# Performance work log

Hardware: AMD Instinct MI355X
Metric: run time of the kernel (lower is better)

The kernel has to match this reference:

```python
import jax, jax.numpy as jnp
import numpy as np

B, L, D = 8, 1024, 512
H, DK, DV = 8, 64, 64
DLAT = 512

def _ln(x, g, b, eps):
    m = jnp.mean(x, axis=-1, keepdims=True)
    var = jnp.mean((x - m) ** 2, axis=-1, keepdims=True)
    return (x - m) * jax.lax.rsqrt(var + eps) * g + b

def setup_inputs() -> dict:
    key = jax.random.key(0)
    ks = jax.random.split(key, 16)
    s = lambda fan: 1.0 / np.sqrt(fan)
    inp = {
        "q": jax.random.normal(ks[0], (B, L, D), jnp.float32),
        "k": jax.random.normal(ks[1], (B, L, D), jnp.float32),
        "v": jax.random.normal(ks[2], (B, L, D), jnp.float32),
        "latent": jax.random.normal(ks[3], (B, 1, DLAT), jnp.float32),
        "Wq": jax.random.normal(ks[4], (D, H * DK), jnp.float32) * s(D),
        "bq": jnp.zeros((H * DK,), jnp.float32),
        "Wk": jax.random.normal(ks[5], (D, H * DK), jnp.float32) * s(D),
        "bk": jnp.zeros((H * DK,), jnp.float32),
        "Wv": jax.random.normal(ks[6], (D, H * DV), jnp.float32) * s(D),
        "bv": jnp.zeros((H * DV,), jnp.float32),
        "Wfc": jax.random.normal(ks[7], (H * DV, D), jnp.float32) * s(H * DV),
        "bfc": jnp.zeros((D,), jnp.float32),
        "Ws1": jax.random.normal(ks[8], (DLAT, 2 * D), jnp.float32) * s(DLAT),
        "bs1": jnp.zeros((2 * D,), jnp.float32),
        "Ws2": jax.random.normal(ks[9], (D, D), jnp.float32) * s(D),
        "bs2": jnp.zeros((D,), jnp.float32),
        "en_g": jnp.ones((D,), jnp.float32),
        "en_b": jnp.zeros((D,), jnp.float32),
        "ln_g": jnp.ones((D,), jnp.float32),
        "ln_b": jnp.zeros((D,), jnp.float32),
    }
    return inp

def reference(q, k, v, latent, Wq, bq, Wk, bk, Wv, bv, Wfc, bfc, Ws1, bs1, Ws2, bs2, en_g, en_b, ln_g, ln_b):
    residual = q
    # QKV projections -> [B, L, H, d]
    Q = (q @ Wq + bq).reshape(B, L, H, DK)
    K = (k @ Wk + bk).reshape(B, L, H, DK)
    V = (v @ Wv + bv).reshape(B, L, H, DV)
    # scaled dot-product attention (dropout = identity in eval)
    scores = jnp.einsum("bqhd,bkhd->bhqk", Q, K) / jnp.sqrt(jnp.float32(DK))
    attn = jax.nn.softmax(scores, axis=-1)
    o = jnp.einsum("bhqk,bkhd->bqhd", attn, V).reshape(B, L, H * DV)
    o = o @ Wfc + bfc
    # ScaledStylizationBlock (FiLM): SiLU -> Linear -> split scale/shift
    lat = jax.nn.silu(latent) @ Ws1 + bs1          # [B, 1, 2D]
    scale, shift = jnp.split(lat, 2, axis=2)
    h = _ln(o, en_g, en_b, 1e-5) * (1.0 + scale) + shift
    h = jax.nn.silu(h) @ Ws2 + bs2
    out = _ln(h + residual, ln_g, ln_b, 1e-6)
    return out, attn
```

## Files before the change

### kernel.cpp

```cpp
#include <hip/hip_runtime.h>
#include <hip/hip_bf16.h>
#include <math.h>

#define BB 8
#define LLEN 1024
#define DDIM 512
#define HH 8
#define DLAT 512
#define NROW (BB * LLEN)
#define ROWELEM 4194304

typedef __bf16 bf16x8 __attribute__((ext_vector_type(8)));
typedef __bf16 bf16x4 __attribute__((ext_vector_type(4)));
typedef float  f32x4  __attribute__((ext_vector_type(4)));

__device__ inline __bf16 f2bf(float f) {
    union { float f; unsigned u; } a; a.f = f;
    unsigned r = (a.u + 0x7fffu + ((a.u >> 16) & 1u)) >> 16;
    union { unsigned short s; __bf16 b; } o; o.s = (unsigned short)r;
    return o.b;
}

__global__ __launch_bounds__(256) void wtrans_kernel(
    const float* __restrict__ W, __bf16* __restrict__ WT)
{
    __shared__ float t[64][65];
    const int tid = threadIdx.x;
    const int bx = blockIdx.x & 7;
    const int by = blockIdx.x >> 3;
    const int r0 = by * 64, c0 = bx * 64;

    #pragma unroll
    for (int p = 0; p < 4; ++p) {
        int r = p * 16 + (tid >> 4);
        int c = (tid & 15) * 4;
        f32x4 v = *(const f32x4*)(W + (size_t)(r0 + r) * 512 + c0 + c);
        t[r][c] = v[0]; t[r][c + 1] = v[1]; t[r][c + 2] = v[2]; t[r][c + 3] = v[3];
    }
    __syncthreads();
    #pragma unroll
    for (int p = 0; p < 4; ++p) {
        int c = p * 16 + (tid >> 4);
        int rc = (tid & 15) * 4;
        bf16x4 o;
        #pragma unroll
        for (int m = 0; m < 4; ++m) o[m] = f2bf(t[rc + m][c]);
        *(bf16x4*)(WT + (size_t)(c0 + c) * 512 + r0 + rc) = o;
    }
}

__global__ __launch_bounds__(256) void wtrans_hilo_kernel(
    const float* __restrict__ W, __bf16* __restrict__ WTh, __bf16* __restrict__ WTl)
{
    __shared__ float t[64][65];
    const int tid = threadIdx.x;
    const int bx = blockIdx.x & 7;
    const int by = blockIdx.x >> 3;
    const int r0 = by * 64, c0 = bx * 64;

    #pragma unroll
    for (int p = 0; p < 4; ++p) {
        int r = p * 16 + (tid >> 4);
        int c = (tid & 15) * 4;
        f32x4 v = *(const f32x4*)(W + (size_t)(r0 + r) * 512 + c0 + c);
        t[r][c] = v[0]; t[r][c + 1] = v[1]; t[r][c + 2] = v[2]; t[r][c + 3] = v[3];
    }
    __syncthreads();
    #pragma unroll
    for (int p = 0; p < 4; ++p) {
        int c = p * 16 + (tid >> 4);
        int rc = (tid & 15) * 4;
        bf16x4 oh, ol;
        #pragma unroll
        for (int m = 0; m < 4; ++m) {
            float v = t[rc + m][c];
            __bf16 hi = f2bf(v);
            oh[m] = hi;
            ol[m] = f2bf(v - (float)hi);
        }
        *(bf16x4*)(WTh + (size_t)(c0 + c) * 512 + r0 + rc) = oh;
        *(bf16x4*)(WTl + (size_t)(c0 + c) * 512 + r0 + rc) = ol;
    }
}

__global__ __launch_bounds__(256) void gemm_qkv_mfma(
    const float* __restrict__ A, const __bf16* __restrict__ Bt,
    const float* __restrict__ bias, __bf16* __restrict__ C)
{
    const int tid  = threadIdx.x;
    const int w    = tid >> 6, lane = tid & 63;
    const int quad = lane >> 4, lid = lane & 15;
    const int wm = w >> 1, wn = w & 1;
    const int col0 = blockIdx.x * 64;
    const int row0 = blockIdx.y * 128;

    __shared__ __bf16 As[128][72];
    __shared__ __bf16 Bs[64][72];

    const f32x4 zero = {0.f, 0.f, 0.f, 0.f};
    f32x4 acc[4][2];
    #pragma unroll
    for (int i = 0; i < 4; ++i)
        #pragma unroll
        for (int j = 0; j < 2; ++j) acc[i][j] = zero;

    for (int kt = 0; kt < 512; kt += 64) {
        __syncthreads();
        {
            const int rr = lane >> 4;
            const int cc = lane & 15;
            #pragma unroll
            for (int p = 0; p < 8; ++p) {
                int r = w * 32 + p * 4 + rr;
                f32x4 v = *(const f32x4*)(A + (size_t)(row0 + r) * 512 + kt + cc * 4);
                bf16x4 o;
                #pragma unroll
                for (int m = 0; m < 4; ++m) o[m] = f2bf(v[m]);
                *(bf16x4*)&As[r][cc * 4] = o;
            }
        }
        {
            const int rr = lane >> 3;
            const int cc = lane & 7;
            #pragma unroll
            for (int p = 0; p < 2; ++p) {
                int r = w * 16 + p * 8 + rr;
                *(bf16x8*)&Bs[r][cc * 8] =
                    *(const bf16x8*)(Bt + (size_t)(col0 + r) * 512 + kt + cc * 8);
            }
        }
        __syncthreads();
        #pragma unroll
        for (int ks = 0; ks < 2; ++ks) {
            bf16x8 a[4], b[2];
            #pragma unroll
            for (int i = 0; i < 4; ++i)
                a[i] = *(const bf16x8*)&As[wm * 64 + i * 16 + lid][ks * 32 + quad * 8];
            #pragma unroll
            for (int j = 0; j < 2; ++j)
                b[j] = *(const bf16x8*)&Bs[wn * 32 + j * 16 + lid][ks * 32 + quad * 8];
            #pragma unroll
            for (int i = 0; i < 4; ++i)
                #pragma unroll
                for (int j = 0; j < 2; ++j)
                    acc[i][j] = __builtin_amdgcn_mfma_f32_16x16x32_bf16(a[i], b[j], acc[i][j], 0, 0, 0);
        }
    }

    float bcol[2];
    #pragma unroll
    for (int j = 0; j < 2; ++j) bcol[j] = bias[col0 + wn * 32 + j * 16 + lid];
    #pragma unroll
    for (int i = 0; i < 4; ++i)
        #pragma unroll
        for (int j = 0; j < 2; ++j) {
            int colg = col0 + wn * 32 + j * 16 + lid;
            #pragma unroll
            for (int r = 0; r < 4; ++r) {
                int rowg = row0 + wm * 64 + i * 16 + quad * 4 + r;
                C[(size_t)rowg * 512 + colg] = f2bf(acc[i][j][r] + bcol[j]);
            }
        }
}

__global__ __launch_bounds__(256) void gemm_split_mfma(
    const __bf16* __restrict__ Ahi, const __bf16* __restrict__ Alo,
    const __bf16* __restrict__ Bth, const __bf16* __restrict__ Btl,
    const float* __restrict__ bias, float* __restrict__ C)
{
    const int tid  = threadIdx.x;
    const int w    = tid >> 6, lane = tid & 63;
    const int quad = lane >> 4, lid = lane & 15;
    const int wm = w >> 1, wn = w & 1;
    const int col0 = blockIdx.x * 64;
    const int row0 = blockIdx.y * 128;

    __shared__ __bf16 Ah[128][72];
    __shared__ __bf16 Al[128][72];
    __shared__ __bf16 Bh[64][72];
    __shared__ __bf16 Bl[64][72];

    const f32x4 zero = {0.f, 0.f, 0.f, 0.f};
    f32x4 acc[4][2];
    #pragma unroll
    for (int i = 0; i < 4; ++i)
        #pragma unroll
        for (int j = 0; j < 2; ++j) acc[i][j] = zero;

    const int rr = lane >> 3, cc = lane & 7;

    for (int kt = 0; kt < 512; kt += 64) {
        __syncthreads();
        #pragma unroll
        for (int p = 0; p < 4; ++p) {
            int r = w * 32 + p * 8 + rr;
            size_t g = (size_t)(row0 + r) * 512 + kt + cc * 8;
            *(bf16x8*)&Ah[r][cc * 8] = *(const bf16x8*)(Ahi + g);
            *(bf16x8*)&Al[r][cc * 8] = *(const bf16x8*)(Alo + g);
        }
        #pragma unroll
        for (int p = 0; p < 2; ++p) {
            int r = w * 16 + p * 8 + rr;
            size_t g = (size_t)(col0 + r) * 512 + kt + cc * 8;
            *(bf16x8*)&Bh[r][cc * 8] = *(const bf16x8*)(Bth + g);
            *(bf16x8*)&Bl[r][cc * 8] = *(const bf16x8*)(Btl + g);
        }
        __syncthreads();
        #pragma unroll
        for (int ks = 0; ks < 2; ++ks) {
            bf16x8 ah[4], al[4], bh[2], bl[2];
            #pragma unroll
            for (int i = 0; i < 4; ++i) {
                ah[i] = *(const bf16x8*)&Ah[wm * 64 + i * 16 + lid][ks * 32 + quad * 8];
                al[i] = *(const bf16x8*)&Al[wm * 64 + i * 16 + lid][ks * 32 + quad * 8];
            }
            #pragma unroll
            for (int j = 0; j < 2; ++j) {
                bh[j] = *(const bf16x8*)&Bh[wn * 32 + j * 16 + lid][ks * 32 + quad * 8];
                bl[j] = *(const bf16x8*)&Bl[wn * 32 + j * 16 + lid][ks * 32 + quad * 8];
            }
            #pragma unroll
            for (int i = 0; i < 4; ++i)
                #pragma unroll
                for (int j = 0; j < 2; ++j) {
                    f32x4 t = __builtin_amdgcn_mfma_f32_16x16x32_bf16(al[i], bh[j], acc[i][j], 0, 0, 0);
                    t = __builtin_amdgcn_mfma_f32_16x16x32_bf16(ah[i], bl[j], t, 0, 0, 0);
                    acc[i][j] = __builtin_amdgcn_mfma_f32_16x16x32_bf16(ah[i], bh[j], t, 0, 0, 0);
                }
        }
    }

    float bcol[2];
    #pragma unroll
    for (int j = 0; j < 2; ++j) bcol[j] = bias[col0 + wn * 32 + j * 16 + lid];
    #pragma unroll
    for (int i = 0; i < 4; ++i)
        #pragma unroll
        for (int j = 0; j < 2; ++j) {
            int colg = col0 + wn * 32 + j * 16 + lid;
            #pragma unroll
            for (int r = 0; r < 4; ++r) {
                int rowg = row0 + wm * 64 + i * 16 + quad * 4 + r;
                C[(size_t)rowg * 512 + colg] = acc[i][j][r] + bcol[j];
            }
        }
}

__global__ __launch_bounds__(256) void vtrans_kernel(
    const __bf16* __restrict__ Vb, __bf16* __restrict__ VtG)
{
    __shared__ __bf16 t[64][72];
    const int tid = threadIdx.x;
    const int lt = blockIdx.x & 15, h = (blockIdx.x >> 4) & 7, b = blockIdx.x >> 7;
    const int rr = tid >> 3, cc = tid & 7;
    #pragma unroll
    for (int p = 0; p < 2; ++p) {
        int r = p * 32 + rr;
        *(bf16x8*)&t[r][cc * 8] =
            *(const bf16x8*)(Vb + (size_t)(b * LLEN + lt * 64 + r) * DDIM + h * 64 + cc * 8);
    }
    __syncthreads();
    #pragma unroll
    for (int p = 0; p < 2; ++p) {
        int d = p * 32 + rr;
        bf16x8 o;
        #pragma unroll
        for (int m = 0; m < 8; ++m) o[m] = t[cc * 8 + m][d];
        *(bf16x8*)(VtG + ((size_t)((b * 8 + h) * 64 + d)) * LLEN + lt * 64 + cc * 8) = o;
    }
}

__global__ __launch_bounds__(256) void film_latent_kernel(
    const float* __restrict__ latent, const float* __restrict__ Ws1,
    const float* __restrict__ bs1, float* __restrict__ film)
{
    __shared__ float sl[DLAT];
    const int b = blockIdx.x;
    const int tid = threadIdx.x;
    #pragma unroll
    for (int l = 0; l < 2; ++l) {
        int k = tid + l * 256;
        float x = latent[b * DLAT + k];
        sl[k] = x / (1.f + __expf(-x));
    }
    __syncthreads();
    int n = blockIdx.y * 256 + tid;
    float acc = bs1[n];
    for (int k = 0; k < DLAT; ++k)
        acc += sl[k] * Ws1[(size_t)k * 1024 + n];
    film[b * 1024 + n] = acc;
}

__global__ __launch_bounds__(256) void attn_mfma_kernel(
    const __bf16* __restrict__ Qb, const __bf16* __restrict__ Kb,
    const __bf16* __restrict__ VtG, float* __restrict__ attn_out,
    __bf16* __restrict__ Ohi, __bf16* __restrict__ Olo)
{
    const int bid = blockIdx.x;
    const int qt = bid & 15;
    const int h  = (bid >> 4) & 7;
    const int b  = bid >> 7;
    const int q0 = qt * 64;
    const int tid = threadIdx.x;
    const int w    = tid >> 6;
    const int lane = tid & 63;
    const int quad = lane >> 4;
    const int lid  = lane & 15;

    __shared__ __bf16 KtS[64][72];
    __shared__ __bf16 VtS[64][72];
    __shared__ __bf16 PtS[4][16][72];

    const int myq = q0 + w * 16 + lid;
    const __bf16* qptr = Qb + (size_t)(b * LLEN + myq) * DDIM + h * 64 + quad * 8;
    const bf16x8 qf0 = *(const bf16x8*)(qptr);
    const bf16x8 qf1 = *(const bf16x8*)(qptr + 32);

    const size_t kbase = (size_t)(b * LLEN) * DDIM + h * 64;
    const size_t vbase = (size_t)((b * 8 + h) * 64) * LLEN;
    const f32x4 zero = {0.f, 0.f, 0.f, 0.f};
    const float C0 = 0.125f;

    float rsum = 0.f;
    for (int kt = 0; kt < 16; ++kt) {
        __syncthreads();
        #pragma unroll
        for (int rep = 0; rep < 2; ++rep) {
            int s = tid + rep * 256;
            int r = s >> 3, c = s & 7;
            *(bf16x8*)&KtS[r][c * 8] =
                *(const bf16x8*)(Kb + kbase + (size_t)(kt * 64 + r) * DDIM + c * 8);
        }
        __syncthreads();
        #pragma unroll
        for (int st = 0; st < 4; ++st) {
            bf16x8 a0 = *(const bf16x8*)&KtS[st * 16 + lid][quad * 8];
            bf16x8 a1 = *(const bf16x8*)&KtS[st * 16 + lid][32 + quad * 8];
            f32x4 c = __builtin_amdgcn_mfma_f32_16x16x32_bf16(a0, qf0, zero, 0, 0, 0);
            c = __builtin_amdgcn_mfma_f32_16x16x32_bf16(a1, qf1, c, 0, 0, 0);
            #pragma unroll
            for (int r = 0; r < 4; ++r) rsum += __expf(C0 * c[r]);
        }
    }
    rsum += __shfl_xor(rsum, 16, 64);
    rsum += __shfl_xor(rsum, 32, 64);
    const float rinv = 1.f / rsum;

    f32x4 oacc[4] = {zero, zero, zero, zero};
    const size_t abase = ((size_t)((b * 8 + h) * LLEN + myq)) * LLEN;

    for (int kt = 0; kt < 16; ++kt) {
        __syncthreads();
        #pragma unroll
        for (int rep = 0; rep < 2; ++rep) {
            int s = tid + rep * 256;
            int r = s >> 3, c = s & 7;
            *(bf16x8*)&KtS[r][c * 8] =
                *(const bf16x8*)(Kb + kbase + (size_t)(kt * 64 + r) * DDIM + c * 8);
            *(bf16x8*)&VtS[r][c * 8] =
                *(const bf16x8*)(VtG + vbase + (size_t)r * LLEN + kt * 64 + c * 8);
        }
        __syncthreads();
        #pragma unroll
        for (int st = 0; st < 4; ++st) {
            bf16x8 a0 = *(const bf16x8*)&KtS[st * 16 + lid][quad * 8];
            bf16x8 a1 = *(const bf16x8*)&KtS[st * 16 + lid][32 + quad * 8];
            f32x4 c = __builtin_amdgcn_mfma_f32_16x16x32_bf16(a0, qf0, zero, 0, 0, 0);
            c = __builtin_amdgcn_mfma_f32_16x16x32_bf16(a1, qf1, c, 0, 0, 0);
            f32x4 p;
            bf16x4 pk;
            #pragma unroll
            for (int r = 0; r < 4; ++r) {
                p[r] = __expf(C0 * c[r]) * rinv;
                pk[r] = f2bf(p[r]);
            }
            *(f32x4*)(attn_out + abase + kt * 64 + st * 16 + quad * 4) = p;
            *(bf16x4*)&PtS[w][lid][st * 16 + quad * 4] = pk;
        }
        __syncthreads();
        #pragma unroll
        for (int kc = 0; kc < 2; ++kc) {
            bf16x8 pa = *(const bf16x8*)&PtS[w][lid][kc * 32 + quad * 8];
            #pragma unroll
            for (int nt = 0; nt < 4; ++nt) {
                bf16x8 vb = *(const bf16x8*)&VtS[nt * 16 + lid][kc * 32 + quad * 8];
                oacc[nt] = __builtin_amdgcn_mfma_f32_16x16x32_bf16(pa, vb, oacc[nt], 0, 0, 0);
            }
        }
    }

    #pragma unroll
    for (int nt = 0; nt < 4; ++nt)
        #pragma unroll
        for (int r = 0; r < 4; ++r) {
            float val = oacc[nt][r];
            __bf16 hi = f2bf(val);
            size_t idx = (size_t)(b * LLEN + q0 + w * 16 + quad * 4 + r) * DDIM + h * 64 + nt * 16 + lid;
            Ohi[idx] = hi;
            Olo[idx] = f2bf(val - (float)hi);
        }
}

__device__ inline void block_reduce2(float& a, float& b) {
    #pragma unroll
    for (int off = 32; off > 0; off >>= 1) {
        a += __shfl_down(a, off, 64);
        b += __shfl_down(b, off, 64);
    }
    __shared__ float wa[4], wb[4];
    int lane = threadIdx.x & 63, w = threadIdx.x >> 6;
    if (lane == 0) { wa[w] = a; wb[w] = b; }
    __syncthreads();
    if (threadIdx.x == 0) {
        wa[0] = wa[0] + wa[1] + wa[2] + wa[3];
        wb[0] = wb[0] + wb[1] + wb[2] + wb[3];
    }
    __syncthreads();
    a = wa[0];
    b = wb[0];
}

__global__ __launch_bounds__(256) void film_ln_kernel(
    const float* __restrict__ X, const float* __restrict__ en_g,
    const float* __restrict__ en_b, const float* __restrict__ film,
    __bf16* __restrict__ HShi, __bf16* __restrict__ HSlo)
{
    const int row = blockIdx.x;
    const int b = row >> 10;
    const int tid = threadIdx.x;
    const size_t base = (size_t)row * DDIM;

    float x0 = X[base + tid];
    float x1 = X[base + 256 + tid];
    float s = x0 + x1;
    float s2 = x0 * x0 + x1 * x1;
    block_reduce2(s, s2);
    float mean = s * (1.f / 512.f);
    float var = s2 * (1.f / 512.f) - mean * mean;
    float inv = rsqrtf(var + 1e-5f);

    #pragma unroll
    for (int l = 0; l < 2; ++l) {
        int d = tid + l * 256;
        float x = (l == 0) ? x0 : x1;
        float nh = (x - mean) * inv * en_g[d] + en_b[d];
        float sc = film[b * 1024 + d];
        float sh = film[b * 1024 + 512 + d];
        float hv = nh * (1.f + sc) + sh;
        float sv = hv / (1.f + __expf(-hv));
        __bf16 hi = f2bf(sv);
        HShi[base + d] = hi;
        HSlo[base + d] = f2bf(sv - (float)hi);
    }
}

__global__ __launch_bounds__(256) void final_ln_kernel(
    const float* __restrict__ H2, const float* __restrict__ resid,
    const float* __restrict__ g, const float* __restrict__ bta,
    float* __restrict__ out)
{
    const int row = blockIdx.x;
    const int tid = threadIdx.x;
    const size_t base = (size_t)row * DDIM;

    float x0 = H2[base + tid] + resid[base + tid];
    float x1 = H2[base + 256 + tid] + resid[base + 256 + tid];
    float s = x0 + x1;
    float s2 = x0 * x0 + x1 * x1;
    block_reduce2(s, s2);
    float mean = s * (1.f / 512.f);
    float var = s2 * (1.f / 512.f) - mean * mean;
    float inv = rsqrtf(var + 1e-6f);

    #pragma unroll
    for (int l = 0; l < 2; ++l) {
        int d = tid + l * 256;
        float x = (l == 0) ? x0 : x1;
        out[base + d] = (x - mean) * inv * g[d] + bta[d];
    }
}

extern "C" void kernel_launch(void* const* d_in, const int* in_sizes, int n_in,
                              void* d_out, int out_size, void* d_ws, size_t ws_size,
                              hipStream_t stream)
{
    const float* q      = (const float*)d_in[0];
    const float* k      = (const float*)d_in[1];
    const float* v      = (const float*)d_in[2];
    const float* latent = (const float*)d_in[3];
    const float* Wq  = (const float*)d_in[4];
    const float* bq  = (const float*)d_in[5];
    const float* Wk  = (const float*)d_in[6];
    const float* bk  = (const float*)d_in[7];
    const float* Wv  = (const float*)d_in[8];
    const float* bv  = (const float*)d_in[9];
    const float* Wfc = (const float*)d_in[10];
    const float* bfc = (const float*)d_in[11];
    const float* Ws1 = (const float*)d_in[12];
    const float* bs1 = (const float*)d_in[13];
    const float* Ws2 = (const float*)d_in[14];
    const float* bs2 = (const float*)d_in[15];
    const float* en_g = (const float*)d_in[16];
    const float* en_b = (const float*)d_in[17];
    const float* ln_g = (const float*)d_in[18];
    const float* ln_b = (const float*)d_in[19];

    float* out  = (float*)d_out;
    float* attn = out + ROWELEM;

    char* ws = (char*)d_ws;
    __bf16* Qb   = (__bf16*)(ws + 0);
    __bf16* Kb   = (__bf16*)(ws + 8388608);
    __bf16* Vb   = (__bf16*)(ws + 16777216);
    __bf16* VtG  = (__bf16*)(ws + 25165824);
    __bf16* Ohi  = (__bf16*)(ws + 33554432);
    __bf16* Olo  = (__bf16*)(ws + 41943040);
    __bf16* WqT  = (__bf16*)(ws + 50331648);
    __bf16* WkT  = (__bf16*)(ws + 50855936);
    __bf16* WvT  = (__bf16*)(ws + 51380224);
    __bf16* WfhT = (__bf16*)(ws + 51904512);
    __bf16* WflT = (__bf16*)(ws + 52428800);
    __bf16* W2hT = (__bf16*)(ws + 52953088);
    __bf16* W2lT = (__bf16*)(ws + 53477376);
    float*  film = (float*)(ws + 54001664);

    float*  F1   = (float*)(ws + 0);
    __bf16* HShi = Ohi;
    __bf16* HSlo = Olo;
    float*  H2   = (float*)(ws + 16777216);

    wtrans_kernel<<<64, 256, 0, stream>>>(Wq, WqT);
    wtrans_kernel<<<64, 256, 0, stream>>>(Wk, WkT);
    wtrans_kernel<<<64, 256, 0, stream>>>(Wv, WvT);
    wtrans_hilo_kernel<<<64, 256, 0, stream>>>(Wfc, WfhT, WflT);
    wtrans_hilo_kernel<<<64, 256, 0, stream>>>(Ws2, W2hT, W2lT);
    film_latent_kernel<<<dim3(BB, 4), 256, 0, stream>>>(latent, Ws1, bs1, film);

    dim3 ggrid(8, 64);
    gemm_qkv_mfma<<<ggrid, 256, 0, stream>>>(q, WqT, bq, Qb);
    gemm_qkv_mfma<<<ggrid, 256, 0, stream>>>(k, WkT, bk, Kb);
    gemm_qkv_mfma<<<ggrid, 256, 0, stream>>>(v, WvT, bv, Vb);
    vtrans_kernel<<<1024, 256, 0, stream>>>(Vb, VtG);

    attn_mfma_kernel<<<1024, 256, 0, stream>>>(Qb, Kb, VtG, attn, Ohi, Olo);

    gemm_split_mfma<<<ggrid, 256, 0, stream>>>(Ohi, Olo, WfhT, WflT, bfc, F1);
    film_ln_kernel<<<NROW, 256, 0, stream>>>(F1, en_g, en_b, film, HShi, HSlo);
    gemm_split_mfma<<<ggrid, 256, 0, stream>>>(HShi, HSlo, W2hT, W2lT, bs2, H2);
    final_ln_kernel<<<NROW, 256, 0, stream>>>(H2, q, ln_g, ln_b, out);
}
```

Baseline: 572.9 us.

## Double-buffer attention K/V tiles, fuse V transpose into GEMM, merge weight prep launches

The attention kernel now double-buffers its K and V shared-memory tiles. The next tile is prefetched into registers while the current one is being computed, which removes one barrier per iteration. The V projection GEMM writes its output already transposed into the per-head layout, so the separate vtrans kernel and the Vb buffer are gone. The weight-transpose launches are merged into batched grids, the split GEMM uses a 32-wide K step with smaller LDS tiles, and the attention-matrix and final outputs use nontemporal stores. The risks are extra LDS use in the attention kernel, which can lower occupancy, and a barrier replaced by a wave-local waitcnt on PtS, which relies on that buffer being private to each wave.

```diff
diff --git a/kernel.cpp b/kernel.cpp
--- a/kernel.cpp
+++ b/kernel.cpp
@@ -21,9 +21,14 @@
     return o.b;
 }
 
-__global__ __launch_bounds__(256) void wtrans_kernel(
-    const float* __restrict__ W, __bf16* __restrict__ WT)
-{
+__global__ __launch_bounds__(256) void wtrans3_kernel(
+    const float* __restrict__ W0, const float* __restrict__ W1,
+    const float* __restrict__ W2, __bf16* __restrict__ T0,
+    __bf16* __restrict__ T1, __bf16* __restrict__ T2)
+{
+    const float* W = (blockIdx.y == 0) ? W0 : (blockIdx.y == 1) ? W1 : W2;
+    __bf16* WT     = (blockIdx.y == 0) ? T0 : (blockIdx.y == 1) ? T1 : T2;
+
     __shared__ float t[64][65];
     const int tid = threadIdx.x;
     const int bx = blockIdx.x & 7;
@@ -49,9 +54,15 @@
     }
 }
 
-__global__ __launch_bounds__(256) void wtrans_hilo_kernel(
-    const float* __restrict__ W, __bf16* __restrict__ WTh, __bf16* __restrict__ WTl)
-{
+__global__ __launch_bounds__(256) void wtrans_hilo2_kernel(
+    const float* __restrict__ W0, const float* __restrict__ W1,
+    __bf16* __restrict__ H0, __bf16* __restrict__ L0,
+    __bf16* __restrict__ H1, __bf16* __restrict__ L1)
+{
+    const float* W  = (blockIdx.y == 0) ? W0 : W1;
+    __bf16* WTh     = (blockIdx.y == 0) ? H0 : H1;
+    __bf16* WTl     = (blockIdx.y == 0) ? L0 : L1;
+
     __shared__ float t[64][65];
     const int tid = threadIdx.x;
     const int bx = blockIdx.x & 7;
@@ -163,10 +174,9 @@
         }
 }
 
-__global__ __launch_bounds__(256) void gemm_split_mfma(
-    const __bf16* __restrict__ Ahi, const __bf16* __restrict__ Alo,
-    const __bf16* __restrict__ Bth, const __bf16* __restrict__ Btl,
-    const float* __restrict__ bias, float* __restrict__ C)
+__global__ __launch_bounds__(256) void gemm_v_mfma(
+    const float* __restrict__ A, const __bf16* __restrict__ Bt,
+    const float* __restrict__ bias, __bf16* __restrict__ VtG)
 {
     const int tid  = threadIdx.x;
     const int w    = tid >> 6, lane = tid & 63;
@@ -175,10 +185,8 @@
     const int col0 = blockIdx.x * 64;
     const int row0 = blockIdx.y * 128;
 
-    __shared__ __bf16 Ah[128][72];
-    __shared__ __bf16 Al[128][72];
-    __shared__ __bf16 Bh[64][72];
-    __shared__ __bf16 Bl[64][72];
+    __shared__ __bf16 As[128][72];
+    __shared__ __bf16 Bs[64][72];
 
     const f32x4 zero = {0.f, 0.f, 0.f, 0.f};
     f32x4 acc[4][2];
@@ -187,47 +195,137 @@
         #pragma unroll
         for (int j = 0; j < 2; ++j) acc[i][j] = zero;
 
-    const int rr = lane >> 3, cc = lane & 7;
-
     for (int kt = 0; kt < 512; kt += 64) {
         __syncthreads();
-        #pragma unroll
-        for (int p = 0; p < 4; ++p) {
-            int r = w * 32 + p * 8 + rr;
+        {
+            const int rr = lane >> 4;
+            const int cc = lane & 15;
+            #pragma unroll
+            for (int p = 0; p < 8; ++p) {
+                int r = w * 32 + p * 4 + rr;
+                f32x4 v = *(const f32x4*)(A + (size_t)(row0 + r) * 512 + kt + cc * 4);
+                bf16x4 o;
+                #pragma unroll
+                for (int m = 0; m < 4; ++m) o[m] = f2bf(v[m]);
+                *(bf16x4*)&As[r][cc * 4] = o;
+            }
+        }
+        {
+            const int rr = lane >> 3;
+            const int cc = lane & 7;
+            #pragma unroll
+            for (int p = 0; p < 2; ++p) {
+                int r = w * 16 + p * 8 + rr;
+                *(bf16x8*)&Bs[r][cc * 8] =
+                    *(const bf16x8*)(Bt + (size_t)(col0 + r) * 512 + kt + cc * 8);
+            }
+        }
+        __syncthreads();
+        #pragma unroll
+        for (int ks = 0; ks < 2; ++ks) {
+            bf16x8 a[4], b[2];
+            #pragma unroll
+            for (int i = 0; i < 4; ++i)
+                a[i] = *(const bf16x8*)&As[wm * 64 + i * 16 + lid][ks * 32 + quad * 8];
+            #pragma unroll
+            for (int j = 0; j < 2; ++j)
+                b[j] = *(const bf16x8*)&Bs[wn * 32 + j * 16 + lid][ks * 32 + quad * 8];
+            #pragma unroll
+            for (int i = 0; i < 4; ++i)
+                #pragma unroll
+                for (int j = 0; j < 2; ++j)
+                    acc[i][j] = __builtin_amdgcn_mfma_f32_16x16x32_bf16(a[i], b[j], acc[i][j], 0, 0, 0);
+        }
+    }
+
+    __syncthreads();
+    __bf16 (*Ts)[136] = (__bf16 (*)[136])(&As[0][0]);
+    float bcol[2];
+    #pragma unroll
+    for (int j = 0; j < 2; ++j) bcol[j] = bias[col0 + wn * 32 + j * 16 + lid];
+    #pragma unroll
+    for (int i = 0; i < 4; ++i)
+        #pragma unroll
+        for (int j = 0; j < 2; ++j) {
+            int d = wn * 32 + j * 16 + lid;
+            #pragma unroll
+            for (int r = 0; r < 4; ++r) {
+                int l = wm * 64 + i * 16 + quad * 4 + r;
+                Ts[d][l] = f2bf(acc[i][j][r] + bcol[j]);
+            }
+        }
+    __syncthreads();
+    const int b = row0 >> 10, l0 = row0 & 1023, h = blockIdx.x;
+    const size_t obase = (size_t)((b * 8 + h) * 64) * LLEN;
+    #pragma unroll
+    for (int p = 0; p < 4; ++p) {
+        int cix = tid + p * 256;
+        int d = cix >> 4, lc = cix & 15;
+        bf16x8 vv = *(const bf16x8*)&Ts[d][lc * 8];
+        *(bf16x8*)(VtG + obase + (size_t)d * LLEN + l0 + lc * 8) = vv;
+    }
+}
+
+__global__ __launch_bounds__(256) void gemm_split_mfma(
+    const __bf16* __restrict__ Ahi, const __bf16* __restrict__ Alo,
+    const __bf16* __restrict__ Bth, const __bf16* __restrict__ Btl,
+    const float* __restrict__ bias, float* __restrict__ C)
+{
+    const int tid  = threadIdx.x;
+    const int w    = tid >> 6, lane = tid & 63;
+    const int quad = lane >> 4, lid = lane & 15;
+    const int wm = w >> 1, wn = w & 1;
+    const int col0 = blockIdx.x * 64;
+    const int row0 = blockIdx.y * 128;
+
+    __shared__ __bf16 Ah[128][40];
+    __shared__ __bf16 Al[128][40];
+    __shared__ __bf16 Bh[64][40];
+    __shared__ __bf16 Bl[64][40];
+
+    const f32x4 zero = {0.f, 0.f, 0.f, 0.f};
+    f32x4 acc[4][2];
+    #pragma unroll
+    for (int i = 0; i < 4; ++i)
+        #pragma unroll
+        for (int j = 0; j < 2; ++j) acc[i][j] = zero;
+
+    for (int kt = 0; kt < 512; kt += 32) {
+        __syncthreads();
+        #pragma unroll
+        for (int p = 0; p < 2; ++p) {
+            int cix = tid + p * 256;
+            int r = cix >> 2, cc = cix & 3;
             size_t g = (size_t)(row0 + r) * 512 + kt + cc * 8;
             *(bf16x8*)&Ah[r][cc * 8] = *(const bf16x8*)(Ahi + g);
             *(bf16x8*)&Al[r][cc * 8] = *(const bf16x8*)(Alo + g);
         }
-        #pragma unroll
-        for (int p = 0; p < 2; ++p) {
-            int r = w * 16 + p * 8 + rr;
+        {
+            int r = tid >> 2, cc = tid & 3;
             size_t g = (size_t)(col0 + r) * 512 + kt + cc * 8;
             *(bf16x8*)&Bh[r][cc * 8] = *(const bf16x8*)(Bth + g);
             *(bf16x8*)&Bl[r][cc * 8] = *(const bf16x8*)(Btl + g);
         }
         __syncthreads();
-        #pragma unroll
-        for (int ks = 0; ks < 2; ++ks) {
-            bf16x8 ah[4], al[4], bh[2], bl[2];
-            #pragma unroll
-            for (int i = 0; i < 4; ++i) {
-                ah[i] = *(const bf16x8*)&Ah[wm * 64 + i * 16 + lid][ks * 32 + quad * 8];
-                al[i] = *(const bf16x8*)&Al[wm * 64 + i * 16 + lid][ks * 32 + quad * 8];
-            }
+        bf16x8 ah[4], al[4], bh[2], bl[2];
+        #pragma unroll
+        for (int i = 0; i < 4; ++i) {
+            ah[i] = *(const bf16x8*)&Ah[wm * 64 + i * 16 + lid][quad * 8];
+            al[i] = *(const bf16x8*)&Al[wm * 64 + i * 16 + lid][quad * 8];
+        }
+        #pragma unroll
+        for (int j = 0; j < 2; ++j) {
+            bh[j] = *(const bf16x8*)&Bh[wn * 32 + j * 16 + lid][quad * 8];
+            bl[j] = *(const bf16x8*)&Bl[wn * 32 + j * 16 + lid][quad * 8];
+        }
+        #pragma unroll
+        for (int i = 0; i < 4; ++i)
             #pragma unroll
             for (int j = 0; j < 2; ++j) {
-                bh[j] = *(const bf16x8*)&Bh[wn * 32 + j * 16 + lid][ks * 32 + quad * 8];
-                bl[j] = *(const bf16x8*)&Bl[wn * 32 + j * 16 + lid][ks * 32 + quad * 8];
-            }
-            #pragma unroll
-            for (int i = 0; i < 4; ++i)
-                #pragma unroll
-                for (int j = 0; j < 2; ++j) {
-                    f32x4 t = __builtin_amdgcn_mfma_f32_16x16x32_bf16(al[i], bh[j], acc[i][j], 0, 0, 0);
-                    t = __builtin_amdgcn_mfma_f32_16x16x32_bf16(ah[i], bl[j], t, 0, 0, 0);
-                    acc[i][j] = __builtin_amdgcn_mfma_f32_16x16x32_bf16(ah[i], bh[j], t, 0, 0, 0);
-                }
-        }
+                f32x4 t = __builtin_amdgcn_mfma_f32_16x16x32_bf16(al[i], bh[j], acc[i][j], 0, 0, 0);
+                t = __builtin_amdgcn_mfma_f32_16x16x32_bf16(ah[i], bl[j], t, 0, 0, 0);
+                acc[i][j] = __builtin_amdgcn_mfma_f32_16x16x32_bf16(ah[i], bh[j], t, 0, 0, 0);
+            }
     }
 
     float bcol[2];
@@ -244,30 +342,6 @@
                 C[(size_t)rowg * 512 + colg] = acc[i][j][r] + bcol[j];
             }
         }
-}
-
-__global__ __launch_bounds__(256) void vtrans_kernel(
-    const __bf16* __restrict__ Vb, __bf16* __restrict__ VtG)
-{
-    __shared__ __bf16 t[64][72];
-    const int tid = threadIdx.x;
-    const int lt = blockIdx.x & 15, h = (blockIdx.x >> 4) & 7, b = blockIdx.x >> 7;
-    const int rr = tid >> 3, cc = tid & 7;
-    #pragma unroll
-    for (int p = 0; p < 2; ++p) {
-        int r = p * 32 + rr;
-        *(bf16x8*)&t[r][cc * 8] =
-            *(const bf16x8*)(Vb + (size_t)(b * LLEN + lt * 64 + r) * DDIM + h * 64 + cc * 8);
-    }
-    __syncthreads();
-    #pragma unroll
-    for (int p = 0; p < 2; ++p) {
-        int d = p * 32 + rr;
-        bf16x8 o;
-        #pragma unroll
-        for (int m = 0; m < 8; ++m) o[m] = t[cc * 8 + m][d];
-        *(bf16x8*)(VtG + ((size_t)((b * 8 + h) * 64 + d)) * LLEN + lt * 64 + cc * 8) = o;
-    }
 }
 
 __global__ __launch_bounds__(256) void film_latent_kernel(
@@ -307,8 +381,8 @@
     const int quad = lane >> 4;
     const int lid  = lane & 15;
 
-    __shared__ __bf16 KtS[64][72];
-    __shared__ __bf16 VtS[64][72];
+    __shared__ __bf16 KtS[2][64][72];
+    __shared__ __bf16 VtS[2][64][72];
     __shared__ __bf16 PtS[4][16][72];
 
     const int myq = q0 + w * 16 + lid;
@@ -321,26 +395,40 @@
     const f32x4 zero = {0.f, 0.f, 0.f, 0.f};
     const float C0 = 0.125f;
 
+    const int sr = tid >> 3;
+    const int sc = tid & 7;
+
+    #pragma unroll
+    for (int rep = 0; rep < 2; ++rep) {
+        int r = sr + rep * 32;
+        *(bf16x8*)&KtS[0][r][sc * 8] =
+            *(const bf16x8*)(Kb + kbase + (size_t)r * DDIM + sc * 8);
+    }
+    __syncthreads();
+
     float rsum = 0.f;
+    int cur = 0;
     for (int kt = 0; kt < 16; ++kt) {
-        __syncthreads();
-        #pragma unroll
-        for (int rep = 0; rep < 2; ++rep) {
-            int s = tid + rep * 256;
-            int r = s >> 3, c = s & 7;
-            *(bf16x8*)&KtS[r][c * 8] =
-                *(const bf16x8*)(Kb + kbase + (size_t)(kt * 64 + r) * DDIM + c * 8);
-        }
-        __syncthreads();
+        bf16x8 kr0, kr1;
+        if (kt < 15) {
+            kr0 = *(const bf16x8*)(Kb + kbase + (size_t)((kt + 1) * 64 + sr) * DDIM + sc * 8);
+            kr1 = *(const bf16x8*)(Kb + kbase + (size_t)((kt + 1) * 64 + sr + 32) * DDIM + sc * 8);
+        }
         #pragma unroll
         for (int st = 0; st < 4; ++st) {
-            bf16x8 a0 = *(const bf16x8*)&KtS[st * 16 + lid][quad * 8];
-            bf16x8 a1 = *(const bf16x8*)&KtS[st * 16 + lid][32 + quad * 8];
+            bf16x8 a0 = *(const bf16x8*)&KtS[cur][st * 16 + lid][quad * 8];
+            bf16x8 a1 = *(const bf16x8*)&KtS[cur][st * 16 + lid][32 + quad * 8];
             f32x4 c = __builtin_amdgcn_mfma_f32_16x16x32_bf16(a0, qf0, zero, 0, 0, 0);
             c = __builtin_amdgcn_mfma_f32_16x16x32_bf16(a1, qf1, c, 0, 0, 0);
             #pragma unroll
             for (int r = 0; r < 4; ++r) rsum += __expf(C0 * c[r]);
         }
+        if (kt < 15) {
+            *(bf16x8*)&KtS[cur ^ 1][sr][sc * 8] = kr0;
+            *(bf16x8*)&KtS[cur ^ 1][sr + 32][sc * 8] = kr1;
+        }
+        __syncthreads();
+        cur ^= 1;
     }
     rsum += __shfl_xor(rsum, 16, 64);
     rsum += __shfl_xor(rsum, 32, 64);
@@ -349,22 +437,29 @@
     f32x4 oacc[4] = {zero, zero, zero, zero};
     const size_t abase = ((size_t)((b * 8 + h) * LLEN + myq)) * LLEN;
 
+    #pragma unroll
+    for (int rep = 0; rep < 2; ++rep) {
+        int r = sr + rep * 32;
+        *(bf16x8*)&KtS[0][r][sc * 8] =
+            *(const bf16x8*)(Kb + kbase + (size_t)r * DDIM + sc * 8);
+        *(bf16x8*)&VtS[0][r][sc * 8] =
+            *(const bf16x8*)(VtG + vbase + (size_t)r * LLEN + sc * 8);
+    }
+    __syncthreads();
+
+    cur = 0;
     for (int kt = 0; kt < 16; ++kt) {
-        __syncthreads();
-        #pragma unroll
-        for (int rep = 0; rep < 2; ++rep) {
-            int s = tid + rep * 256;
-            int r = s >> 3, c = s & 7;
-            *(bf16x8*)&KtS[r][c * 8] =
-                *(const bf16x8*)(Kb + kbase + (size_t)(kt * 64 + r) * DDIM + c * 8);
-            *(bf16x8*)&VtS[r][c * 8] =
-                *(const bf16x8*)(VtG + vbase + (size_t)r * LLEN + kt * 64 + c * 8);
-        }
-        __syncthreads();
+        bf16x8 kr0, kr1, vr0, vr1;
+        if (kt < 15) {
+            kr0 = *(const bf16x8*)(Kb + kbase + (size_t)((kt + 1) * 64 + sr) * DDIM + sc * 8);
+            kr1 = *(const bf16x8*)(Kb + kbase + (size_t)((kt + 1) * 64 + sr + 32) * DDIM + sc * 8);
+            vr0 = *(const bf16x8*)(VtG + vbase + (size_t)sr * LLEN + (kt + 1) * 64 + sc * 8);
+            vr1 = *(const bf16x8*)(VtG + vbase + (size_t)(sr + 32) * LLEN + (kt + 1) * 64 + sc * 8);
+        }
         #pragma unroll
         for (int st = 0; st < 4; ++st) {
-            bf16x8 a0 = *(const bf16x8*)&KtS[st * 16 + lid][quad * 8];
-            bf16x8 a1 = *(const bf16x8*)&KtS[st * 16 + lid][32 + quad * 8];
+            bf16x8 a0 = *(const bf16x8*)&KtS[cur][st * 16 + lid][quad * 8];
+            bf16x8 a1 = *(const bf16x8*)&KtS[cur][st * 16 + lid][32 + quad * 8];
             f32x4 c = __builtin_amdgcn_mfma_f32_16x16x32_bf16(a0, qf0, zero, 0, 0, 0);
             c = __builtin_amdgcn_mfma_f32_16x16x32_bf16(a1, qf1, c, 0, 0, 0);
             f32x4 p;
@@ -374,19 +469,27 @@
                 p[r] = __expf(C0 * c[r]) * rinv;
                 pk[r] = f2bf(p[r]);
             }
-            *(f32x4*)(attn_out + abase + kt * 64 + st * 16 + quad * 4) = p;
+            __builtin_nontemporal_store(p, (f32x4*)(attn_out + abase + kt * 64 + st * 16 + quad * 4));
             *(bf16x4*)&PtS[w][lid][st * 16 + quad * 4] = pk;
         }
-        __syncthreads();
+        asm volatile("s_waitcnt lgkmcnt(0)" ::: "memory");
         #pragma unroll
         for (int kc = 0; kc < 2; ++kc) {
             bf16x8 pa = *(const bf16x8*)&PtS[w][lid][kc * 32 + quad * 8];
             #pragma unroll
             for (int nt = 0; nt < 4; ++nt) {
-                bf16x8 vb = *(const bf16x8*)&VtS[nt * 16 + lid][kc * 32 + quad * 8];
+                bf16x8 vb = *(const bf16x8*)&VtS[cur][nt * 16 + lid][kc * 32 + quad * 8];
                 oacc[nt] = __builtin_amdgcn_mfma_f32_16x16x32_bf16(pa, vb, oacc[nt], 0, 0, 0);
             }
         }
+        if (kt < 15) {
+            *(bf16x8*)&KtS[cur ^ 1][sr][sc * 8] = kr0;
+            *(bf16x8*)&KtS[cur ^ 1][sr + 32][sc * 8] = kr1;
+            *(bf16x8*)&VtS[cur ^ 1][sr][sc * 8] = vr0;
+            *(bf16x8*)&VtS[cur ^ 1][sr + 32][sc * 8] = vr1;
+        }
+        __syncthreads();
+        cur ^= 1;
     }
 
     #pragma unroll
@@ -476,7 +579,8 @@
     for (int l = 0; l < 2; ++l) {
         int d = tid + l * 256;
         float x = (l == 0) ? x0 : x1;
-        out[base + d] = (x - mean) * inv * g[d] + bta[d];
+        float o = (x - mean) * inv * g[d] + bta[d];
+        __builtin_nontemporal_store(o, out + base + d);
     }
 }
 
@@ -511,36 +615,31 @@
     char* ws = (char*)d_ws;
     __bf16* Qb   = (__bf16*)(ws + 0);
     __bf16* Kb   = (__bf16*)(ws + 8388608);
-    __bf16* Vb   = (__bf16*)(ws + 16777216);
-    __bf16* VtG  = (__bf16*)(ws + 25165824);
-    __bf16* Ohi  = (__bf16*)(ws + 33554432);
-    __bf16* Olo  = (__bf16*)(ws + 41943040);
-    __bf16* WqT  = (__bf16*)(ws + 50331648);
-    __bf16* WkT  = (__bf16*)(ws + 50855936);
-    __bf16* WvT  = (__bf16*)(ws + 51380224);
-    __bf16* WfhT = (__bf16*)(ws + 51904512);
-    __bf16* WflT = (__bf16*)(ws + 52428800);
-    __bf16* W2hT = (__bf16*)(ws + 52953088);
-    __bf16* W2lT = (__bf16*)(ws + 53477376);
-    float*  film = (float*)(ws + 54001664);
+    __bf16* VtG  = (__bf16*)(ws + 16777216);
+    __bf16* Ohi  = (__bf16*)(ws + 25165824);
+    __bf16* Olo  = (__bf16*)(ws + 33554432);
+    __bf16* WqT  = (__bf16*)(ws + 41943040);
+    __bf16* WkT  = (__bf16*)(ws + 42467328);
+    __bf16* WvT  = (__bf16*)(ws + 42991616);
+    __bf16* WfhT = (__bf16*)(ws + 43515904);
+    __bf16* WflT = (__bf16*)(ws + 44040192);
+    __bf16* W2hT = (__bf16*)(ws + 44564480);
+    __bf16* W2lT = (__bf16*)(ws + 45088768);
+    float*  film = (float*)(ws + 45613056);
 
     float*  F1   = (float*)(ws + 0);
     __bf16* HShi = Ohi;
     __bf16* HSlo = Olo;
-    float*  H2   = (float*)(ws + 16777216);
-
-    wtrans_kernel<<<64, 256, 0, stream>>>(Wq, WqT);
-    wtrans_kernel<<<64, 256, 0, stream>>>(Wk, WkT);
-    wtrans_kernel<<<64, 256, 0, stream>>>(Wv, WvT);
-    wtrans_hilo_kernel<<<64, 256, 0, stream>>>(Wfc, WfhT, WflT);
-    wtrans_hilo_kernel<<<64, 256, 0, stream>>>(Ws2, W2hT, W2lT);
+    float*  H2   = (float*)(ws + 0);
+
+    wtrans3_kernel<<<dim3(64, 3), 256, 0, stream>>>(Wq, Wk, Wv, WqT, WkT, WvT);
+    wtrans_hilo2_kernel<<<dim3(64, 2), 256, 0, stream>>>(Wfc, Ws2, WfhT, WflT, W2hT, W2lT);
     film_latent_kernel<<<dim3(BB, 4), 256, 0, stream>>>(latent, Ws1, bs1, film);
 
     dim3 ggrid(8, 64);
     gemm_qkv_mfma<<<ggrid, 256, 0, stream>>>(q, WqT, bq, Qb);
     gemm_qkv_mfma<<<ggrid, 256, 0, stream>>>(k, WkT, bk, Kb);
-    gemm_qkv_mfma<<<ggrid, 256, 0, stream>>>(v, WvT, bv, Vb);
-    vtrans_kernel<<<1024, 256, 0, stream>>>(Vb, VtG);
+    gemm_v_mfma<<<ggrid, 256, 0, stream>>>(v, WvT, bv, VtG);
 
     attn_mfma_kernel<<<1024, 256, 0, stream>>>(Qb, Kb, VtG, attn, Ohi, Olo);
 
```

After: 578.4 us. Within noise of the previous version (+1.0%).
